# Performance work log

Hardware: AMD Instinct MI355X
Metric: run time of the kernel (lower is better)

Reference implementation:

```python
import jax, jax.numpy as jnp
import numpy as np

D = 1024

def setup_inputs() -> dict:
    key = jax.random.key(0)
    ks = jax.random.split(key, 7)
    s = D ** -0.5
    return {
        "x": jax.random.normal(ks[0], (8, 2048, D), dtype=jnp.float32),
        "Wq": jax.random.normal(ks[1], (D, D), dtype=jnp.float32) * s,
        "bq": jax.random.normal(ks[2], (D,), dtype=jnp.float32) * 0.02,
        "Wk": jax.random.normal(ks[3], (D, D), dtype=jnp.float32) * s,
        "bk": jax.random.normal(ks[4], (D,), dtype=jnp.float32) * 0.02,
        "Wv": jax.random.normal(ks[5], (D, D), dtype=jnp.float32) * s,
        "bv": jax.random.normal(ks[6], (D,), dtype=jnp.float32) * 0.02,
    }

def reference(x, Wq, bq, Wk, bk, Wv, bv):
    # torch nn.Linear: y = x @ W.T + b; here W stored as (D_in, D_out) directly.
    scaling = jnp.asarray(D, x.dtype) ** -0.5
    q = (jnp.einsum('btd,de->bte', x, Wq) + bq) * scaling
    k = jnp.einsum('btd,de->bte', x, Wk) + bk
    v = jnp.einsum('btd,de->bte', x, Wv) + bv
    attn = jax.nn.softmax(jnp.einsum('bqd,bkd->bqk', q, k), axis=-1)
    return jnp.einsum('bqk,bkd->bqd', attn, v)
```

## Files before the change

kernel.cpp:

```cpp
#include <hip/hip_runtime.h>

typedef unsigned short u16;
typedef __attribute__((ext_vector_type(8))) short short8;
typedef __attribute__((ext_vector_type(4))) float f32x4;
typedef __attribute__((ext_vector_type(4))) float f4;
typedef __attribute__((ext_vector_type(4))) unsigned short u16x4;

#define AS3 __attribute__((address_space(3)))
#define AS1 __attribute__((address_space(1)))

static __device__ __forceinline__ u16 f2b(float f) {
  unsigned int u = __builtin_bit_cast(unsigned int, f);
  u += 0x7FFFu + ((u >> 16) & 1u);
  return (u16)(u >> 16);
}

__global__ void k_cvt_x(const float* __restrict__ x, u16* __restrict__ xb, int n4) {
  int i = blockIdx.x * blockDim.x + threadIdx.x;
  int stride = gridDim.x * blockDim.x;
  for (; i < n4; i += stride) {
    f4 v = ((const f4*)x)[i];
    u16x4 o = { f2b(v[0]), f2b(v[1]), f2b(v[2]), f2b(v[3]) };
    ((u16x4*)xb)[i] = o;
  }
}

__global__ __launch_bounds__(256) void k_trans_w(const float* __restrict__ Wq,
                                                 const float* __restrict__ Wk,
                                                 const float* __restrict__ Wv,
                                                 u16* __restrict__ Wt) {
  __shared__ float t[32][33];
  int z = blockIdx.z;
  const float* W = z == 0 ? Wq : (z == 1 ? Wk : Wv);
  float scale = z == 0 ? 0.03125f : 1.0f;
  int kb = blockIdx.y * 32, nb = blockIdx.x * 32;
  int tx = threadIdx.x & 31, ty = threadIdx.x >> 5;
#pragma unroll
  for (int i = 0; i < 4; i++) {
    int r = ty + i * 8;
    t[r][tx] = W[(long long)(kb + r) * 1024 + nb + tx];
  }
  __syncthreads();
#pragma unroll
  for (int i = 0; i < 4; i++) {
    int r = ty + i * 8;
    Wt[(long long)(z * 1024 + nb + r) * 1024 + kb + tx] = f2b(t[tx][r] * scale);
  }
}

__global__ void k_bias(const float* __restrict__ bq, const float* __restrict__ bk,
                       const float* __restrict__ bv, float* __restrict__ bcat) {
  int i = blockIdx.x * 256 + threadIdx.x;
  if (i < 1024) bcat[i] = bq[i] * 0.03125f;
  else if (i < 2048) bcat[i] = bk[i - 1024];
  else if (i < 3072) bcat[i] = bv[i - 2048];
}

__global__ void k_zero(float* __restrict__ p, int n) {
  int i = blockIdx.x * 256 + threadIdx.x;
  if (i < n) p[i] = 0.0f;
}

__global__ __launch_bounds__(256) void k_trans_v(const u16* __restrict__ V, u16* __restrict__ Vt) {
  __shared__ u16 t[64][65];
  int b = blockIdx.z;
  int tb = blockIdx.x * 64, db = blockIdx.y * 64;
  int tx = threadIdx.x & 63, ty = threadIdx.x >> 6;
  const u16* Vi = V + (long long)b * 2048 * 1024;
  u16* Vo = Vt + (long long)b * 1024 * 2048;
#pragma unroll
  for (int i = 0; i < 16; i++) {
    int r = ty + i * 4;
    t[r][tx] = Vi[(long long)(tb + r) * 1024 + db + tx];
  }
  __syncthreads();
#pragma unroll
  for (int i = 0; i < 16; i++) {
    int r = ty + i * 4;
    Vo[(long long)(db + r) * 2048 + tb + tx] = t[tx][r];
  }
}


#define STAGE_U(MATBASE, GPTR, d_, ks_, kt_) do {                              \
    _Pragma("unroll")                                                          \
    for (int q_ = 0; q_ < 2; ++q_) {                                           \
      const u16* gp_ = (GPTR) + goff[q_] + (kt_) * 64 + (ks_) * 32;            \
      __builtin_amdgcn_global_load_lds((const AS1 void*)gp_,                   \
          (AS3 void*)(sm + (MATBASE) + ((d_) * 2 + (ks_)) * 16384 +            \
                      (wave * 2 + q_) * 1024), 16, 0, 0);                      \
    }                                                                          \
  } while (0)

#define PHASE(d_, ks_, mh_, STG, VM_) do {                                     \
    AS3 char* Asl_ = sm + ((d_) * 2 + (ks_)) * 16384;                          \
    AS3 char* Bsl_ = sm + 65536 + ((d_) * 2 + (ks_)) * 16384;                  \
    if ((mh_) == 0) {                                                          \
      _Pragma("unroll")                                                        \
      for (int nf_ = 0; nf_ < 4; ++nf_)                                        \
        bfr[nf_] = *(const AS3 short8*)(Bsl_ + boff[nf_]);                     \
    }                                                                          \
    _Pragma("unroll")                                                          \
    for (int mf_ = 0; mf_ < 4; ++mf_)                                          \
      afr[mf_] = *(const AS3 short8*)(Asl_ + aoff[mh_][mf_]);                  \
    STG;                                                                       \
    __builtin_amdgcn_s_barrier();                                              \
    __builtin_amdgcn_sched_barrier(0);                                         \
    __builtin_amdgcn_s_setprio(1);                                             \
    _Pragma("unroll")                                                          \
    for (int mf_ = 0; mf_ < 4; ++mf_)                                          \
      _Pragma("unroll")                                                        \
      for (int nf_ = 0; nf_ < 4; ++nf_)                                        \
        acc[(mh_) * 4 + mf_][nf_] = __builtin_amdgcn_mfma_f32_16x16x32_bf16(   \
            afr[mf_], bfr[nf_], acc[(mh_) * 4 + mf_][nf_], 0, 0, 0);           \
    __builtin_amdgcn_s_setprio(0);                                             \
    if (VM_) asm volatile("s_waitcnt vmcnt(4)" ::: "memory");                  \
    __builtin_amdgcn_s_barrier();                                              \
    __builtin_amdgcn_sched_barrier(0);                                         \
  } while (0)

template <int KD>
static __device__ __forceinline__ void gemm256(const u16* __restrict__ A,
                                               const u16* __restrict__ B,
                                               AS3 char* sm, f32x4 acc[8][4]) {
  constexpr int NT = KD / 64;
  const int tid = threadIdx.x, lane = tid & 63, wave = tid >> 6;
  const int wm = wave >> 2, wn = wave & 3;

  int goff[2];
#pragma unroll
  for (int q = 0; q < 2; ++q) {
    int P = (wave * 2 + q) * 1024 + lane * 16;
    int pr = P >> 6, pc = (P >> 4) & 3;
    int lc = pc ^ ((pr >> 1) & 3);
    goff[q] = pr * KD + lc * 8;
  }
  int aoff[2][4], boff[4];
#pragma unroll
  for (int mh = 0; mh < 2; ++mh)
#pragma unroll
    for (int mf = 0; mf < 4; ++mf) {
      int r = wm * 128 + mh * 64 + mf * 16 + (lane & 15);
      aoff[mh][mf] = r * 64 + ((((lane >> 4) ^ ((r >> 1) & 3))) << 4);
    }
#pragma unroll
  for (int nf = 0; nf < 4; ++nf) {
    int r = wn * 64 + nf * 16 + (lane & 15);
    boff[nf] = r * 64 + ((((lane >> 4) ^ ((r >> 1) & 3))) << 4);
  }

  short8 afr[4], bfr[4];

  STAGE_U(0, A, 0, 0, 0);
  STAGE_U(65536, B, 0, 0, 0);
  STAGE_U(0, A, 0, 1, 0);
  STAGE_U(65536, B, 0, 1, 0);
  STAGE_U(0, A, 1, 0, 1);
  STAGE_U(65536, B, 1, 0, 1);
  asm volatile("s_waitcnt vmcnt(4)" ::: "memory");
  __builtin_amdgcn_s_barrier();
  __builtin_amdgcn_sched_barrier(0);

  for (int i = 0; i < NT / 2; ++i) {
    int t1 = 2 * i + 1;
    int t2 = 2 * i + 2 < NT ? 2 * i + 2 : 0;
    int t3 = 2 * i + 3 < NT ? 2 * i + 3 : 1;
    PHASE(0, 0, 0, STAGE_U(0, A, 1, 1, t1), 0);
    PHASE(0, 0, 1, STAGE_U(65536, B, 1, 1, t1), 0);
    PHASE(0, 1, 0, STAGE_U(0, A, 0, 0, t2), 0);
    PHASE(0, 1, 1, STAGE_U(65536, B, 0, 0, t2), 1);
    PHASE(1, 0, 0, STAGE_U(0, A, 0, 1, t2), 0);
    PHASE(1, 0, 1, STAGE_U(65536, B, 0, 1, t2), 0);
    PHASE(1, 1, 0, STAGE_U(0, A, 1, 0, t3), 0);
    PHASE(1, 1, 1, STAGE_U(65536, B, 1, 0, t3), 1);
  }
  asm volatile("s_waitcnt vmcnt(0)" ::: "memory");
  __builtin_amdgcn_s_barrier();
}

__global__ __launch_bounds__(512, 2) void k_qkv256(const u16* __restrict__ xb,
                                                   const u16* __restrict__ Wt,
                                                   const float* __restrict__ bcat,
                                                   u16* __restrict__ Qb, u16* __restrict__ Kb,
                                                   u16* __restrict__ Vb) {
  extern __shared__ char smem_raw[];
  AS3 char* sm = (AS3 char*)smem_raw;
  int nx = gridDim.x;
  int id = blockIdx.y * nx + blockIdx.x;
  int qq = (nx * gridDim.y) >> 3;
  int nid = (id & 7) * qq + (id >> 3);
  int bx = nid % nx, by = nid / nx;
  const u16* A = xb + (long long)by * 256 * 1024;
  const u16* B = Wt + (long long)bx * 256 * 1024;
  f32x4 acc[8][4] = {};
  gemm256<1024>(A, B, sm, acc);
  int lane = threadIdx.x & 63, wave = threadIdx.x >> 6;
  int wm = wave >> 2, wn = wave & 3;
  int which = bx >> 2;
  u16* out = which == 0 ? Qb : (which == 1 ? Kb : Vb);
#pragma unroll
  for (int mf = 0; mf < 8; ++mf)
#pragma unroll
    for (int nf = 0; nf < 4; ++nf) {
      int colg = bx * 256 + wn * 64 + nf * 16 + (lane & 15);
      float bia = bcat[colg];
      int d = colg & 1023;
#pragma unroll
      for (int r = 0; r < 4; ++r) {
        int row = by * 256 + wm * 128 + mf * 16 + ((lane >> 4) << 2) + r;
        out[(long long)row * 1024 + d] = f2b(acc[mf][nf][r] + bia);
      }
    }
}

__global__ __launch_bounds__(512, 2) void k_qk256(const u16* __restrict__ Qb,
                                                  const u16* __restrict__ Kb,
                                                  u16* __restrict__ P, float* __restrict__ rsum,
                                                  int bbase, long long pStride) {
  extern __shared__ char smem_raw[];
  AS3 char* sm = (AS3 char*)smem_raw;
  int b = bbase + blockIdx.z;
  int nx = gridDim.x;
  int id = blockIdx.y * nx + blockIdx.x;
  int qq = (nx * gridDim.y) >> 3;
  int nid = (id & 7) * qq + (id >> 3);
  int bx = nid % nx, by = nid / nx;
  const u16* A = Qb + (long long)b * 2048 * 1024 + (long long)by * 256 * 1024;
  const u16* B = Kb + (long long)b * 2048 * 1024 + (long long)bx * 256 * 1024;
  f32x4 acc[8][4] = {};
  gemm256<1024>(A, B, sm, acc);
  u16* Pb = P + (long long)blockIdx.z * pStride;
  float* rs = rsum + (long long)b * 2048;
  int lane = threadIdx.x & 63, wave = threadIdx.x >> 6;
  int wm = wave >> 2, wn = wave & 3;
#pragma unroll
  for (int mf = 0; mf < 8; ++mf)
#pragma unroll
    for (int r = 0; r < 4; ++r) {
      int row = by * 256 + wm * 128 + mf * 16 + ((lane >> 4) << 2) + r;
      float s = 0.0f;
#pragma unroll
      for (int nf = 0; nf < 4; ++nf) {
        float e = __expf(acc[mf][nf][r]);
        Pb[(long long)row * 2048 + bx * 256 + wn * 64 + nf * 16 + (lane & 15)] = f2b(e);
        s += e;
      }
      s += __shfl_xor(s, 1);
      s += __shfl_xor(s, 2);
      s += __shfl_xor(s, 4);
      s += __shfl_xor(s, 8);
      if ((lane & 15) == 0) atomicAdd(&rs[row], s);
    }
}

__global__ __launch_bounds__(512, 2) void k_pv256(const u16* __restrict__ P,
                                                  const u16* __restrict__ Vt,
                                                  const float* __restrict__ rsum,
                                                  float* __restrict__ out,
                                                  int bbase, long long pStride) {
  extern __shared__ char smem_raw[];
  AS3 char* sm = (AS3 char*)smem_raw;
  int b = bbase + blockIdx.z;
  int nx = gridDim.x;
  int id = blockIdx.y * nx + blockIdx.x;
  int qq = (nx * gridDim.y) >> 3;
  int nid = (id & 7) * qq + (id >> 3);
  int bx = nid % nx, by = nid / nx;
  const u16* A = P + (long long)blockIdx.z * pStride + (long long)by * 256 * 2048;
  const u16* B = Vt + (long long)b * 1024 * 2048 + (long long)bx * 256 * 2048;
  f32x4 acc[8][4] = {};
  gemm256<2048>(A, B, sm, acc);
  float* ob = out + (long long)b * 2048 * 1024;
  const float* rs = rsum + (long long)b * 2048;
  int lane = threadIdx.x & 63, wave = threadIdx.x >> 6;
  int wm = wave >> 2, wn = wave & 3;
#pragma unroll
  for (int mf = 0; mf < 8; ++mf)
#pragma unroll
    for (int r = 0; r < 4; ++r) {
      int row = by * 256 + wm * 128 + mf * 16 + ((lane >> 4) << 2) + r;
      float inv = 1.0f / rs[row];
#pragma unroll
      for (int nf = 0; nf < 4; ++nf) {
        ob[(long long)row * 1024 + bx * 256 + wn * 64 + nf * 16 + (lane & 15)] =
            acc[mf][nf][r] * inv;
      }
    }
}

extern "C" void kernel_launch(void* const* d_in, const int* in_sizes, int n_in,
                              void* d_out, int out_size, void* d_ws, size_t ws_size,
                              hipStream_t stream) {
  const float* x = (const float*)d_in[0];
  const float* Wq = (const float*)d_in[1];
  const float* bq = (const float*)d_in[2];
  const float* Wk = (const float*)d_in[3];
  const float* bk = (const float*)d_in[4];
  const float* Wv = (const float*)d_in[5];
  const float* bv = (const float*)d_in[6];
  float* out = (float*)d_out;
  char* ws = (char*)d_ws;

  const long long B = 8, T = 2048, D = 1024, BT = B * T;

  size_t off = 0;
  auto alloc = [&](size_t bytes) {
    size_t r = off;
    off += (bytes + 255) & ~(size_t)255;
    return r;
  };
  size_t oXB = alloc(BT * D * 2);
  size_t oWT = alloc((size_t)3072 * 1024 * 2);
  size_t oBC = alloc(3072 * 4);
  size_t oQ = alloc(BT * D * 2);
  size_t oK = alloc(BT * D * 2);
  size_t oV = alloc(BT * D * 2);
  size_t oVT = alloc(BT * D * 2);
  size_t oRS = alloc(BT * 4);
  size_t oP = off;
  bool batched = ws_size >= off + (size_t)B * T * T * 2;

  u16* xb = (u16*)(ws + oXB);
  u16* Wt = (u16*)(ws + oWT);
  float* bcat = (float*)(ws + oBC);
  u16* Qb = (u16*)(ws + oQ);
  u16* Kb = (u16*)(ws + oK);
  u16* Vb = (u16*)(ws + oV);
  u16* Vt = (u16*)(ws + oVT);
  float* rsum = (float*)(ws + oRS);
  u16* P = (u16*)(ws + oP);

  (void)hipFuncSetAttribute((const void*)k_qkv256, hipFuncAttributeMaxDynamicSharedMemorySize, 131072);
  (void)hipFuncSetAttribute((const void*)k_qk256, hipFuncAttributeMaxDynamicSharedMemorySize, 131072);
  (void)hipFuncSetAttribute((const void*)k_pv256, hipFuncAttributeMaxDynamicSharedMemorySize, 131072);

  k_cvt_x<<<dim3(2048), dim3(256), 0, stream>>>(x, xb, (int)(BT * D / 4));
  k_trans_w<<<dim3(32, 32, 3), dim3(256), 0, stream>>>(Wq, Wk, Wv, Wt);
  k_bias<<<dim3(12), dim3(256), 0, stream>>>(bq, bk, bv, bcat);
  k_qkv256<<<dim3(12, 64, 1), dim3(512), 131072, stream>>>(xb, Wt, bcat, Qb, Kb, Vb);
  k_trans_v<<<dim3(32, 16, 8), dim3(256), 0, stream>>>(Vb, Vt);
  k_zero<<<dim3(64), dim3(256), 0, stream>>>(rsum, (int)BT);

  if (batched) {
    k_qk256<<<dim3(8, 8, 8), dim3(512), 131072, stream>>>(Qb, Kb, P, rsum, 0, T * T);
    k_pv256<<<dim3(4, 8, 8), dim3(512), 131072, stream>>>(P, Vt, rsum, out, 0, T * T);
  } else {
    for (int b = 0; b < 8; b++) {
      k_qk256<<<dim3(8, 8, 1), dim3(512), 131072, stream>>>(Qb, Kb, P, rsum, b, 0);
      k_pv256<<<dim3(4, 8, 1), dim3(512), 131072, stream>>>(P, Vt, rsum, out, b, 0);
    }
  }
}
```

Before: 402.8 us.

## Fuse prep kernels into one launch and write V transposed from QKV epilogue

Merges the x conversion, weight transpose, bias concat and rsum zeroing into a single k_prep kernel, which cuts four launches to one. It also drops the separate V transpose kernel: the QKV GEMM epilogue for the V columns now writes 4-element vectors straight into the transposed Vt layout. This removes a 32MB read-and-write round trip and one launch. The cost is strided scattered stores of 8 bytes each in the V epilogue, and a __syncthreads inside one branch of the prep kernel, which is safe only because that branch is uniform per block.

```diff
diff --git a/kernel.cpp b/kernel.cpp
--- a/kernel.cpp
+++ b/kernel.cpp
@@ -15,69 +15,56 @@
   return (u16)(u >> 16);
 }
 
-__global__ void k_cvt_x(const float* __restrict__ x, u16* __restrict__ xb, int n4) {
-  int i = blockIdx.x * blockDim.x + threadIdx.x;
-  int stride = gridDim.x * blockDim.x;
-  for (; i < n4; i += stride) {
-    f4 v = ((const f4*)x)[i];
-    u16x4 o = { f2b(v[0]), f2b(v[1]), f2b(v[2]), f2b(v[3]) };
-    ((u16x4*)xb)[i] = o;
-  }
-}
-
-__global__ __launch_bounds__(256) void k_trans_w(const float* __restrict__ Wq,
-                                                 const float* __restrict__ Wk,
-                                                 const float* __restrict__ Wv,
-                                                 u16* __restrict__ Wt) {
+__global__ __launch_bounds__(256) void k_prep(const float* __restrict__ x,
+                                              const float* __restrict__ Wq,
+                                              const float* __restrict__ Wk,
+                                              const float* __restrict__ Wv,
+                                              const float* __restrict__ bq,
+                                              const float* __restrict__ bk,
+                                              const float* __restrict__ bv,
+                                              u16* __restrict__ xb,
+                                              u16* __restrict__ Wt,
+                                              float* __restrict__ bcat,
+                                              float* __restrict__ rsum) {
   __shared__ float t[32][33];
-  int z = blockIdx.z;
-  const float* W = z == 0 ? Wq : (z == 1 ? Wk : Wv);
-  float scale = z == 0 ? 0.03125f : 1.0f;
-  int kb = blockIdx.y * 32, nb = blockIdx.x * 32;
-  int tx = threadIdx.x & 31, ty = threadIdx.x >> 5;
-#pragma unroll
-  for (int i = 0; i < 4; i++) {
-    int r = ty + i * 8;
-    t[r][tx] = W[(long long)(kb + r) * 1024 + nb + tx];
-  }
-  __syncthreads();
-#pragma unroll
-  for (int i = 0; i < 4; i++) {
-    int r = ty + i * 8;
-    Wt[(long long)(z * 1024 + nb + r) * 1024 + kb + tx] = f2b(t[tx][r] * scale);
-  }
-}
-
-__global__ void k_bias(const float* __restrict__ bq, const float* __restrict__ bk,
-                       const float* __restrict__ bv, float* __restrict__ bcat) {
-  int i = blockIdx.x * 256 + threadIdx.x;
-  if (i < 1024) bcat[i] = bq[i] * 0.03125f;
-  else if (i < 2048) bcat[i] = bk[i - 1024];
-  else if (i < 3072) bcat[i] = bv[i - 2048];
-}
-
-__global__ void k_zero(float* __restrict__ p, int n) {
-  int i = blockIdx.x * 256 + threadIdx.x;
-  if (i < n) p[i] = 0.0f;
-}
-
-__global__ __launch_bounds__(256) void k_trans_v(const u16* __restrict__ V, u16* __restrict__ Vt) {
-  __shared__ u16 t[64][65];
-  int b = blockIdx.z;
-  int tb = blockIdx.x * 64, db = blockIdx.y * 64;
-  int tx = threadIdx.x & 63, ty = threadIdx.x >> 6;
-  const u16* Vi = V + (long long)b * 2048 * 1024;
-  u16* Vo = Vt + (long long)b * 1024 * 2048;
-#pragma unroll
-  for (int i = 0; i < 16; i++) {
-    int r = ty + i * 4;
-    t[r][tx] = Vi[(long long)(tb + r) * 1024 + db + tx];
-  }
-  __syncthreads();
-#pragma unroll
-  for (int i = 0; i < 16; i++) {
-    int r = ty + i * 4;
-    Vo[(long long)(db + r) * 2048 + tb + tx] = t[tx][r];
+  int bid = blockIdx.x, tid = threadIdx.x;
+  if (bid < 2048) {
+    const int n4 = 8 * 2048 * 1024 / 4;
+    int i = bid * 256 + tid;
+    const int stride = 2048 * 256;
+#pragma unroll 2
+    for (; i < n4; i += stride) {
+      f4 v = ((const f4*)x)[i];
+      u16x4 o = { f2b(v[0]), f2b(v[1]), f2b(v[2]), f2b(v[3]) };
+      ((u16x4*)xb)[i] = o;
+    }
+  } else if (bid < 5120) {
+    int wi = bid - 2048;
+    int z = wi >> 10;
+    int r2 = wi & 1023;
+    int kb = (r2 >> 5) * 32, nb = (r2 & 31) * 32;
+    const float* W = z == 0 ? Wq : (z == 1 ? Wk : Wv);
+    float scale = z == 0 ? 0.03125f : 1.0f;
+    int tx = tid & 31, ty = tid >> 5;
+#pragma unroll
+    for (int i = 0; i < 4; i++) {
+      int r = ty + i * 8;
+      t[r][tx] = W[(long long)(kb + r) * 1024 + nb + tx];
+    }
+    __syncthreads();
+#pragma unroll
+    for (int i = 0; i < 4; i++) {
+      int r = ty + i * 8;
+      Wt[(long long)(z * 1024 + nb + r) * 1024 + kb + tx] = f2b(t[tx][r] * scale);
+    }
+  } else if (bid < 5132) {
+    int i = (bid - 5120) * 256 + tid;
+    if (i < 1024) bcat[i] = bq[i] * 0.03125f;
+    else if (i < 2048) bcat[i] = bk[i - 1024];
+    else if (i < 3072) bcat[i] = bv[i - 2048];
+  } else {
+    int i = (bid - 5132) * 256 + tid;
+    if (i < 16384) rsum[i] = 0.0f;
   }
 }
 
@@ -182,7 +169,7 @@
                                                    const u16* __restrict__ Wt,
                                                    const float* __restrict__ bcat,
                                                    u16* __restrict__ Qb, u16* __restrict__ Kb,
-                                                   u16* __restrict__ Vb) {
+                                                   u16* __restrict__ Vt) {
   extern __shared__ char smem_raw[];
   AS3 char* sm = (AS3 char*)smem_raw;
   int nx = gridDim.x;
@@ -197,20 +184,37 @@
   int lane = threadIdx.x & 63, wave = threadIdx.x >> 6;
   int wm = wave >> 2, wn = wave & 3;
   int which = bx >> 2;
-  u16* out = which == 0 ? Qb : (which == 1 ? Kb : Vb);
-#pragma unroll
-  for (int mf = 0; mf < 8; ++mf)
-#pragma unroll
-    for (int nf = 0; nf < 4; ++nf) {
-      int colg = bx * 256 + wn * 64 + nf * 16 + (lane & 15);
-      float bia = bcat[colg];
-      int d = colg & 1023;
-#pragma unroll
-      for (int r = 0; r < 4; ++r) {
-        int row = by * 256 + wm * 128 + mf * 16 + ((lane >> 4) << 2) + r;
-        out[(long long)row * 1024 + d] = f2b(acc[mf][nf][r] + bia);
+  if (which < 2) {
+    u16* out = which == 0 ? Qb : Kb;
+#pragma unroll
+    for (int mf = 0; mf < 8; ++mf)
+#pragma unroll
+      for (int nf = 0; nf < 4; ++nf) {
+        int colg = bx * 256 + wn * 64 + nf * 16 + (lane & 15);
+        float bia = bcat[colg];
+        int d = colg & 1023;
+#pragma unroll
+        for (int r = 0; r < 4; ++r) {
+          int row = by * 256 + wm * 128 + mf * 16 + ((lane >> 4) << 2) + r;
+          out[(long long)row * 1024 + d] = f2b(acc[mf][nf][r] + bia);
+        }
       }
-    }
+  } else {
+    int b = (by * 256) >> 11;
+    u16* vt = Vt + (long long)b * 1024 * 2048;
+    int t0 = ((by * 256) & 2047) + wm * 128 + ((lane >> 4) << 2);
+#pragma unroll
+    for (int mf = 0; mf < 8; ++mf)
+#pragma unroll
+      for (int nf = 0; nf < 4; ++nf) {
+        int colg = bx * 256 + wn * 64 + nf * 16 + (lane & 15);
+        float bia = bcat[colg];
+        int d = colg & 1023;
+        u16x4 o = { f2b(acc[mf][nf][0] + bia), f2b(acc[mf][nf][1] + bia),
+                    f2b(acc[mf][nf][2] + bia), f2b(acc[mf][nf][3] + bia) };
+        *(u16x4*)&vt[(long long)d * 2048 + t0 + mf * 16] = o;
+      }
+  }
 }
 
 __global__ __launch_bounds__(512, 2) void k_qk256(const u16* __restrict__ Qb,
@@ -314,7 +318,6 @@
   size_t oBC = alloc(3072 * 4);
   size_t oQ = alloc(BT * D * 2);
   size_t oK = alloc(BT * D * 2);
-  size_t oV = alloc(BT * D * 2);
   size_t oVT = alloc(BT * D * 2);
   size_t oRS = alloc(BT * 4);
   size_t oP = off;
@@ -325,7 +328,6 @@
   float* bcat = (float*)(ws + oBC);
   u16* Qb = (u16*)(ws + oQ);
   u16* Kb = (u16*)(ws + oK);
-  u16* Vb = (u16*)(ws + oV);
   u16* Vt = (u16*)(ws + oVT);
   float* rsum = (float*)(ws + oRS);
   u16* P = (u16*)(ws + oP);
@@ -334,12 +336,8 @@
   (void)hipFuncSetAttribute((const void*)k_qk256, hipFuncAttributeMaxDynamicSharedMemorySize, 131072);
   (void)hipFuncSetAttribute((const void*)k_pv256, hipFuncAttributeMaxDynamicSharedMemorySize, 131072);
 
-  k_cvt_x<<<dim3(2048), dim3(256), 0, stream>>>(x, xb, (int)(BT * D / 4));
-  k_trans_w<<<dim3(32, 32, 3), dim3(256), 0, stream>>>(Wq, Wk, Wv, Wt);
-  k_bias<<<dim3(12), dim3(256), 0, stream>>>(bq, bk, bv, bcat);
-  k_qkv256<<<dim3(12, 64, 1), dim3(512), 131072, stream>>>(xb, Wt, bcat, Qb, Kb, Vb);
-  k_trans_v<<<dim3(32, 16, 8), dim3(256), 0, stream>>>(Vb, Vt);
-  k_zero<<<dim3(64), dim3(256), 0, stream>>>(rsum, (int)BT);
+  k_prep<<<dim3(5196), dim3(256), 0, stream>>>(x, Wq, Wk, Wv, bq, bk, bv, xb, Wt, bcat, rsum);
+  k_qkv256<<<dim3(12, 64, 1), dim3(512), 131072, stream>>>(xb, Wt, bcat, Qb, Kb, Vt);
 
   if (batched) {
     k_qk256<<<dim3(8, 8, 8), dim3(512), 131072, stream>>>(Qb, Kb, P, rsum, 0, T * T);
```

Result: faster. 388.4 us (-3.6%).
